# Kernel optimization log

Hardware: AMD Instinct MI355X
Metric: run time of the kernel (lower is better)

Reference implementation:

```python
import jax, jax.numpy as jnp
import numpy as np


def _patchify(x, p):
    # x: [B, V, H, W] -> [B, V, L, p*p] with L = (H/p)*(W/p), matching Conv2d(kernel=stride=p)
    B, V, H, W = x.shape
    hp, wp = H // p, W // p
    x = x.reshape(B, V, hp, p, wp, p)
    x = x.transpose(0, 1, 2, 4, 3, 5)  # [B, V, hp, wp, p, p]
    return x.reshape(B, V, hp * wp, p * p)


def setup_inputs() -> dict:
    key = jax.random.key(0)
    ks = jax.random.split(key, 12)
    B, V, H, W, p, D = 2, 16, 128, 256, 4, 1024
    L = (H // p) * (W // p)  # 2048
    std = 0.02
    return {
        "x": jax.random.normal(ks[0], (B, V, H, W), jnp.float32),
        "proj_w": jax.random.normal(ks[1], (V, D, p * p), jnp.float32) * std,
        "proj_b": jnp.zeros((V, D), jnp.float32),
        "channel_embed": jax.random.normal(ks[2], (1, V, D), jnp.float32) * std,
        "pos_embed": jax.random.normal(ks[3], (1, L, D), jnp.float32) * std,
        "channel_query": jax.random.normal(ks[4], (1, 1, D), jnp.float32) * std,
        "wq": jax.random.normal(ks[5], (D, D), jnp.float32) * std,
        "wk": jax.random.normal(ks[6], (D, D), jnp.float32) * std,
        "wv": jax.random.normal(ks[7], (D, D), jnp.float32) * std,
        "bq": jnp.zeros((D,), jnp.float32),
        "bk": jnp.zeros((D,), jnp.float32),
        "bv": jnp.zeros((D,), jnp.float32),
        "wo": jax.random.normal(ks[8], (D, D), jnp.float32) * std,
        "bo": jnp.zeros((D,), jnp.float32),
        "num_heads": 16,
    }


def reference(x, proj_w, proj_b, channel_embed, pos_embed, channel_query,
              wq, wk, wv, bq, bk, bv, wo, bo, num_heads):
    D = proj_w.shape[1]
    p = int(round(np.sqrt(proj_w.shape[-1])))
    nh = int(num_heads)
    dh = D // nh

    # per-variable patch embed (Conv2d k=stride=p == patch-matmul)
    patches = _patchify(x, p)                                   # [B, V, L, p*p]
    tok = jnp.einsum('bvlk,vdk->bvld', patches, proj_w)         # [B, V, L, D]
    tok = tok + proj_b[None, :, None, :]

    # add variable (channel) and positional embeddings
    tok = tok + channel_embed[:, :, None, :] + pos_embed[:, None, :, :]

    # aggregate_variables: single-query MHA over V, batched over B*L
    h = tok.transpose(0, 2, 1, 3)                               # [B, L, V, D]
    q = channel_query[0, 0] @ wq.T + bq                         # [D]
    qh = q.reshape(nh, dh)
    k = (jnp.einsum('blvd,ed->blve', h, wk) + bk).reshape(*h.shape[:3], nh, dh)
    v = (jnp.einsum('blvd,ed->blve', h, wv) + bv).reshape(*h.shape[:3], nh, dh)
    scores = jnp.einsum('he,blvhe->blhv', qh, k) / np.sqrt(dh)  # [B, L, nh, V]
    attn = jax.nn.softmax(scores, axis=-1)
    ctx = jnp.einsum('blhv,blvhe->blhe', attn, v)               # [B, L, nh, dh]
    ctx = ctx.reshape(h.shape[0], h.shape[1], D)
    out = ctx @ wo.T + bo                                       # [B, L, D]
    return out
```

## Files before the change

kernel.cpp:

```cpp
#include <hip/hip_runtime.h>
#include <hip/hip_bf16.h>

using bf16 = __hip_bfloat16;
using bf16x8 = __attribute__((ext_vector_type(8))) short;
using f32x4  = __attribute__((ext_vector_type(4))) float;

__device__ inline unsigned short f2bu(float f){ bf16 h = __float2bfloat16(f); return *(unsigned short*)&h; }
__device__ inline void async_cp16(const void* g, void* l){
  __builtin_amdgcn_global_load_lds((const __attribute__((address_space(1))) void*)g,
                                   (__attribute__((address_space(3))) void*)l, 16, 0, 0);
}
union BF8 { unsigned short s[8]; bf16x8 v; };

constexpr int D_ = 1024, L_ = 2048;
constexpr int CN = 384;

__device__ inline size_t w3idx(int row, int col){
  const int hh = row >> 6, m = row & 15, dt = (row >> 4) & 3;
  const int vp = col >> 5, quad = (col >> 3) & 3, j = col & 7;
  return (size_t)hh*18432 + vp*2048 + dt*512 + quad*128 + m*8 + j;
}

__global__ __launch_bounds__(256) void k_prep2(const float* __restrict__ wv, const float* __restrict__ wo,
                                               const float* __restrict__ pe,
                                               const float* __restrict__ proj_w, const float* __restrict__ proj_b,
                                               const float* __restrict__ ce, const float* __restrict__ cq,
                                               const float* __restrict__ wq, const float* __restrict__ bq,
                                               const float* __restrict__ wk,
                                               unsigned short* __restrict__ Ab, unsigned short* __restrict__ wo_b,
                                               unsigned short* __restrict__ pe_b,
                                               unsigned short* __restrict__ Btb){
  __shared__ float t[64][17];
  __shared__ float qL[64];
  __shared__ float red[4][64];
  const int blk = blockIdx.x;
  const int tid = threadIdx.x;
  if (blk < 4096){
    int i = blk*256 + tid;
    const float* src; unsigned short* dst; size_t off;
    if (i < 262144){ src = wv; dst = Ab;   off = i; }
    else if (i < 524288){ src = wo; dst = wo_b; off = i - 262144; }
    else           { src = pe; dst = pe_b; off = i - 524288; }
    float4 v = *(const float4*)(src + off*4);
    *(ushort4*)(dst + off*4) = make_ushort4(f2bu(v.x), f2bu(v.y), f2bu(v.z), f2bu(v.w));
  } else if (blk < 4352){
    const int r_ = blk - 4096;
    const int v = r_ >> 4, dd0 = (r_ & 15)*64;
    { const int r = tid >> 2, kq = tid & 3;
      float4 a = *(const float4*)(proj_w + ((size_t)(v*D_ + dd0 + r))*16 + kq*4);
      t[r][kq*4+0]=a.x; t[r][kq*4+1]=a.y; t[r][kq*4+2]=a.z; t[r][kq*4+3]=a.w; }
    __syncthreads();
    { const int k = tid >> 4, c0 = (tid & 15)*4;
      ushort4 o = make_ushort4(f2bu(t[c0+0][k]), f2bu(t[c0+1][k]), f2bu(t[c0+2][k]), f2bu(t[c0+3][k]));
      *(ushort4*)(Btb + (size_t)(v*16+k)*D_ + dd0 + c0) = o; }
    if (tid < 16){
      const int c0 = tid*4;
      float4 pb = *(const float4*)(proj_b + v*D_ + dd0 + c0);
      float4 cc = *(const float4*)(ce     + v*D_ + dd0 + c0);
      ushort4 o = make_ushort4(f2bu(pb.x+cc.x), f2bu(pb.y+cc.y), f2bu(pb.z+cc.z), f2bu(pb.w+cc.w));
      *(ushort4*)(Btb + (size_t)(256+v)*D_ + dd0 + c0) = o;
    }
  } else {
    const int b = blk - 4352;
    const int hh = b >> 4, dq = b & 15;
    const int wave = tid >> 6, lane = tid & 63;
    {
      float cqv[16];
      #pragma unroll
      for (int k=0;k<16;++k) cqv[k] = cq[lane + 64*k];
      #pragma unroll
      for (int j=0;j<16;++j){
        const int e = hh*64 + wave*16 + j;
        const float* wr = wq + (size_t)e*D_;
        float p = 0.f;
        #pragma unroll
        for (int k=0;k<16;++k) p += cqv[k]*wr[lane + 64*k];
        #pragma unroll
        for (int m=32;m>=1;m>>=1) p += __shfl_xor(p, m, 64);
        if (lane==0) qL[wave*16+j] = p + bq[e];
      }
    }
    __syncthreads();
    {
      const int eg = wave, dl = lane;
      const int d = dq*64 + dl;
      float s = 0.f;
      #pragma unroll
      for (int j=0;j<16;++j){
        int e = hh*64 + eg*16 + j;
        s += qL[eg*16+j]*wk[(size_t)e*D_ + d];
      }
      red[eg][dl] = s;
      __syncthreads();
      if (eg==0)
        Ab[(size_t)(1024+hh)*D_ + d] = f2bu(((red[0][dl]+red[1][dl]) + (red[2][dl]+red[3][dl]))*0.125f);
    }
  }
}

template<int MFRAG, bool BIAS, bool WB2>
__device__ inline void gemm_body(unsigned short* As, unsigned short* Bs,
                                 const unsigned short* __restrict__ Abf, const unsigned short* __restrict__ Bt,
                                 const float* __restrict__ bias, float* __restrict__ C,
                                 unsigned short* __restrict__ W, const float* __restrict__ bvp,
                                 int m0, int n0, int K, int ldc, int Mvalid){
  const int tid = threadIdx.x;
  const int wave = tid >> 6, lane = tid & 63;
  const int wm = wave & 1, wn = wave >> 1;
  const int lm = lane & 15, kg4 = lane >> 4;
  f32x4 acc[MFRAG][4];
  #pragma unroll
  for (int mf=0;mf<MFRAG;++mf)
    #pragma unroll
    for (int nf=0;nf<4;++nf) acc[mf][nf] = (f32x4){0.f,0.f,0.f,0.f};
  for (int k0=0; k0<K; k0+=64){
    #pragma unroll
    for (int i=0;i<MFRAG;++i){
      int idx = i*256 + tid;
      int row = idx >> 3, g = (idx & 7) ^ (row & 7);
      async_cp16(Abf + (size_t)(m0+row)*K + k0 + g*8, &As[idx*8]);
    }
    #pragma unroll
    for (int i=0;i<4;++i){
      int idx = i*256 + tid;
      int row = idx >> 3, g = (idx & 7) ^ (row & 7);
      async_cp16(Bt + (size_t)(n0+row)*K + k0 + g*8, &Bs[idx*8]);
    }
    __syncthreads();
    #pragma unroll
    for (int c=0;c<2;++c){
      bf16x8 af[MFRAG], bfr[4];
      #pragma unroll
      for (int f=0;f<MFRAG;++f){
        int row = wm*16*MFRAG + f*16 + lm;
        af[f] = *(const bf16x8*)(&As[row*64 + (((c*4+kg4) ^ (row&7)))*8]);
      }
      #pragma unroll
      for (int f=0;f<4;++f){
        int colr = wn*64 + f*16 + lm;
        bfr[f] = *(const bf16x8*)(&Bs[colr*64 + (((c*4+kg4) ^ (colr&7)))*8]);
      }
      #pragma unroll
      for (int mf=0;mf<MFRAG;++mf)
        #pragma unroll
        for (int nf=0;nf<4;++nf)
          acc[mf][nf] = __builtin_amdgcn_mfma_f32_16x16x32_bf16(af[mf], bfr[nf], acc[mf][nf], 0,0,0);
    }
    __syncthreads();
  }
  #pragma unroll
  for (int nf=0;nf<4;++nf){
    int col = n0 + wn*64 + nf*16 + lm;
    float bval = BIAS ? bias[col] : 0.f;
    #pragma unroll
    for (int mf=0;mf<MFRAG;++mf){
      #pragma unroll
      for (int r=0;r<4;++r){
        int row = m0 + wm*16*MFRAG + mf*16 + kg4*4 + r;
        if (row < Mvalid){
          float v = acc[mf][nf][r];
          C[(size_t)row*ldc + col] = v + bval;
          if (WB2 && row < 1024){
            if (col < 256)      W[w3idx(row,col)] = f2bu(v);
            else if (col < 272) W[w3idx(row,col)] = f2bu(v + bvp[row]);
            else if (col < 288) W[w3idx(row,col)] = 0;
          }
        }
      }
    }
  }
}

__global__ __launch_bounds__(256) void k_gemmCP2(const unsigned short* __restrict__ Ab,
                                                 const unsigned short* __restrict__ Btb,
                                                 const unsigned short* __restrict__ pe_b,
                                                 const float* __restrict__ bv,
                                                 float* __restrict__ Cbig, unsigned short* __restrict__ Wb2,
                                                 float* __restrict__ P2){
  __shared__ unsigned short As[64*64];
  __shared__ unsigned short Bs[128*64];
  if (blockIdx.x < 51){
    int bx = blockIdx.x % 3, by = blockIdx.x / 3;
    gemm_body<2,false,true>(As, Bs, Ab, Btb, nullptr, Cbig, Wb2, bv, by*64, bx*128, 1024, CN, 1040);
  } else {
    int b = blockIdx.x - 51;
    int bx = b & 7, by = b >> 3;
    gemm_body<1,false,false>(As, Bs, pe_b, Ab, nullptr, P2, nullptr, nullptr, by*32, bx*128, 1024, 1024, 2048);
  }
}

__global__ __launch_bounds__(256) void k_gemmOut(const unsigned short* __restrict__ ctxF,
                                                 const unsigned short* __restrict__ wo_b,
                                                 const float* __restrict__ bo, float* __restrict__ C){
  __shared__ unsigned short As[64*64];
  __shared__ unsigned short Bs[128*64];
  gemm_body<2,true,false>(As, Bs, ctxF, wo_b, bo, C, nullptr, nullptr,
                          blockIdx.y*64, blockIdx.x*128, 1024, 1024, 4096);
}

__global__ __launch_bounds__(256) void k_fused9(const float* __restrict__ x,
                                                const float* __restrict__ Cbig,
                                                const unsigned short* __restrict__ W3,
                                                const float* __restrict__ P2,
                                                unsigned short* __restrict__ ctxF){
  __shared__ float patchP[16*260];
  __shared__ float attnT[4*320];
  __shared__ __align__(16) unsigned short S[16*264];
  const int tid = threadIdx.x;
  const int bb  = blockIdx.x >> 9;
  const int sg  = (blockIdx.x >> 2) & 127;
  const int hqq = blockIdx.x & 3;
  unsigned short* ctx = ctxF + (size_t)bb*L_*D_;
  const int l0 = sg*16;
  {
    const int v = tid >> 4, u = tid & 15;
    const int hi = l0 >> 6, wi0 = l0 & 63;
    const float* xp = x + ((size_t)((bb*16+v)*128 + hi*4)*256 + (wi0+u)*4);
    float* dst = &patchP[u*260 + v*16];
    #pragma unroll
    for (int pi=0; pi<4; ++pi){
      float4 r = *(const float4*)(xp + pi*256);
      dst[pi*4+0]=r.x; dst[pi*4+1]=r.y; dst[pi*4+2]=r.z; dst[pi*4+3]=r.w;
    }
  }
  __syncthreads();
  if (tid < 64){
    const int s = tid >> 2, h4 = tid & 3;
    const int hh = hqq*4 + h4;
    const float* qrow = Cbig + (size_t)(1024+hh)*CN;
    const float* prow = &patchP[s*260];
    float4 qc0 = *(const float4*)(qrow+256);
    float4 qc1 = *(const float4*)(qrow+260);
    float4 qc2 = *(const float4*)(qrow+264);
    float4 qc3 = *(const float4*)(qrow+268);
    float qcv[16] = {qc0.x,qc0.y,qc0.z,qc0.w, qc1.x,qc1.y,qc1.z,qc1.w,
                     qc2.x,qc2.y,qc2.z,qc2.w, qc3.x,qc3.y,qc3.z,qc3.w};
    float sc[16];
    #pragma unroll
    for (int v=0; v<16; ++v){
      const float* qp = qrow + v*16;
      const float* pp = prow + v*16;
      float4 qa = *(const float4*)(qp+0),  qb = *(const float4*)(qp+4);
      float4 qc = *(const float4*)(qp+8),  qd = *(const float4*)(qp+12);
      float4 pa = *(const float4*)(pp+0),  pb2 = *(const float4*)(pp+4);
      float4 pc = *(const float4*)(pp+8),  pd = *(const float4*)(pp+12);
      float a = qcv[v];
      a += qa.x*pa.x + qa.y*pa.y + qa.z*pa.z + qa.w*pa.w;
      a += qb.x*pb2.x + qb.y*pb2.y + qb.z*pb2.z + qb.w*pb2.w;
      a += qc.x*pc.x + qc.y*pc.y + qc.z*pc.z + qc.w*pc.w;
      a += qd.x*pd.x + qd.y*pd.y + qd.z*pd.z + qd.w*pd.w;
      sc[v] = a;
    }
    float mx = sc[0];
    #pragma unroll
    for (int v=1;v<16;++v) mx = fmaxf(mx, sc[v]);
    float sum = 0.f;
    #pragma unroll
    for (int v=0;v<16;++v){ sc[v] = __expf(sc[v]-mx); sum += sc[v]; }
    float inv = 1.f/sum;
    float* arow = &attnT[h4*320 + s*20];
    #pragma unroll
    for (int v=0;v<16;++v) arow[v] = sc[v]*inv;
  }
  __syncthreads();
  const int wave = tid >> 6, lane = tid & 63;
  const int m = lane & 15, quad = lane >> 4;
  const int hh = hqq*4 + wave;
  const float* at = &attnT[wave*320];
  const unsigned short* wbase = W3 + (size_t)hh*18432 + lane*8;
  f32x4 acc[4];
  #pragma unroll
  for (int dt=0;dt<4;++dt) acc[dt] = (f32x4){0.f,0.f,0.f,0.f};
  #pragma unroll
  for (int vp=0; vp<9; ++vp){
    BF8 af;
    if (vp < 8){
      const int v = vp*2 + (quad>>1);
      const int k8 = (quad&1)*8;
      const float aw = at[m*20 + v];
      const float* pp = &patchP[m*260 + v*16 + k8];
      float4 p0 = *(const float4*)(pp+0);
      float4 p1 = *(const float4*)(pp+4);
      af.s[0]=f2bu(aw*p0.x); af.s[1]=f2bu(aw*p0.y); af.s[2]=f2bu(aw*p0.z); af.s[3]=f2bu(aw*p0.w);
      af.s[4]=f2bu(aw*p1.x); af.s[5]=f2bu(aw*p1.y); af.s[6]=f2bu(aw*p1.z); af.s[7]=f2bu(aw*p1.w);
    } else {
      #pragma unroll
      for (int j=0;j<8;++j)
        af.s[j] = (quad < 2) ? f2bu(at[m*20 + quad*8 + j]) : (unsigned short)0;
    }
    #pragma unroll
    for (int dt=0; dt<4; ++dt){
      const bf16x8 bf = *(const bf16x8*)(wbase + vp*2048 + dt*512);
      acc[dt] = __builtin_amdgcn_mfma_f32_16x16x32_bf16(af.v, bf, acc[dt], 0,0,0);
    }
  }
  const int dblk0 = wave*64;
  #pragma unroll
  for (int dt=0; dt<4; ++dt){
    const int d = hqq*256 + dblk0 + dt*16 + m;
    #pragma unroll
    for (int r=0;r<4;++r){
      const int s = quad*4 + r;
      S[s*264 + dblk0 + dt*16 + m] = f2bu(acc[dt][r] + P2[(size_t)(l0+s)*D_ + d]);
    }
  }
  __syncthreads();
  {
    const int row = tid >> 4, ch = tid & 15;
    const unsigned short* srcp = &S[row*264 + ch*16];
    unsigned short* dstp = ctx + (size_t)(l0+row)*D_ + hqq*256 + ch*16;
    *(uint4*)(dstp)   = *(const uint4*)(srcp);
    *(uint4*)(dstp+8) = *(const uint4*)(srcp+8);
  }
}

extern "C" void kernel_launch(void* const* d_in, const int* in_sizes, int n_in,
                              void* d_out, int out_size, void* d_ws, size_t ws_size,
                              hipStream_t stream){
  const float* x      = (const float*)d_in[0];
  const float* proj_w = (const float*)d_in[1];
  const float* proj_b = (const float*)d_in[2];
  const float* ce     = (const float*)d_in[3];
  const float* pe     = (const float*)d_in[4];
  const float* cq     = (const float*)d_in[5];
  const float* wq     = (const float*)d_in[6];
  const float* wk     = (const float*)d_in[7];
  const float* wv     = (const float*)d_in[8];
  const float* bq     = (const float*)d_in[9];
  const float* bv     = (const float*)d_in[11];
  const float* wo     = (const float*)d_in[12];
  const float* bo     = (const float*)d_in[13];
  float* out = (float*)d_out;

  char* base = (char*)d_ws;
  unsigned short* Ab   = (unsigned short*)(base);
  unsigned short* Btb  = (unsigned short*)(base + 2359296);
  float*          Cbig = (float*)(base + 3145728);
  unsigned short* wo_b = (unsigned short*)(base + 4743168);
  unsigned short* Wb2  = (unsigned short*)(base + 6840320);
  float*          P2   = (float*)(base + 7430144);
  unsigned short* ctxF = (unsigned short*)(base + 15818752);
  unsigned short* pe_b = (unsigned short*)(base + 24207360);

  k_prep2<<<4608, 256, 0, stream>>>(wv, wo, pe, proj_w, proj_b, ce, cq, wq, bq, wk, Ab, wo_b, pe_b, Btb);
  k_gemmCP2<<<563, 256, 0, stream>>>(Ab, Btb, pe_b, bv, Cbig, Wb2, P2);
  k_fused9<<<1024, 256, 0, stream>>>(x, Cbig, Wb2, P2, ctxF);
  k_gemmOut<<<dim3(8,64), 256, 0, stream>>>(ctxF, wo_b, bo, out);
}
```

Before: 173.8 us.

## Merge four head-quarter blocks into one 1024-thread block per token group

The fused attention kernel now runs one 1024-thread block per 16-token group covering all 16 heads, instead of four 256-thread blocks that each handled four heads. Each x patch tile is loaded once per group rather than four times, and every thread issues a single float4 load. The trade-off is a drop from 1024 to 256 blocks with larger shared-memory use per block. That may lower occupancy and leave only one block per CU on a 256-CU device.

```diff
diff --git a/kernel.cpp b/kernel.cpp
--- a/kernel.cpp
+++ b/kernel.cpp
@@ -198,36 +198,31 @@
                           blockIdx.y*64, blockIdx.x*128, 1024, 1024, 4096);
 }
 
-__global__ __launch_bounds__(256) void k_fused9(const float* __restrict__ x,
-                                                const float* __restrict__ Cbig,
-                                                const unsigned short* __restrict__ W3,
-                                                const float* __restrict__ P2,
-                                                unsigned short* __restrict__ ctxF){
+__global__ __launch_bounds__(1024) void k_fused10(const float* __restrict__ x,
+                                                  const float* __restrict__ Cbig,
+                                                  const unsigned short* __restrict__ W3,
+                                                  const float* __restrict__ P2,
+                                                  unsigned short* __restrict__ ctxF){
   __shared__ float patchP[16*260];
-  __shared__ float attnT[4*320];
-  __shared__ __align__(16) unsigned short S[16*264];
+  __shared__ float attnT[16*320];
+  __shared__ __align__(16) unsigned short S[16*1032];
   const int tid = threadIdx.x;
-  const int bb  = blockIdx.x >> 9;
-  const int sg  = (blockIdx.x >> 2) & 127;
-  const int hqq = blockIdx.x & 3;
+  const int bb  = blockIdx.x >> 7;
+  const int sg  = blockIdx.x & 127;
   unsigned short* ctx = ctxF + (size_t)bb*L_*D_;
   const int l0 = sg*16;
   {
-    const int v = tid >> 4, u = tid & 15;
+    const int u = tid & 15, pi = (tid >> 4) & 3, v = tid >> 6;
     const int hi = l0 >> 6, wi0 = l0 & 63;
-    const float* xp = x + ((size_t)((bb*16+v)*128 + hi*4)*256 + (wi0+u)*4);
-    float* dst = &patchP[u*260 + v*16];
-    #pragma unroll
-    for (int pi=0; pi<4; ++pi){
-      float4 r = *(const float4*)(xp + pi*256);
-      dst[pi*4+0]=r.x; dst[pi*4+1]=r.y; dst[pi*4+2]=r.z; dst[pi*4+3]=r.w;
-    }
+    const float* xp = x + ((size_t)((bb*16+v)*128 + hi*4 + pi)*256 + (wi0+u)*4);
+    float4 r = *(const float4*)xp;
+    float* dst = &patchP[u*260 + v*16 + pi*4];
+    dst[0]=r.x; dst[1]=r.y; dst[2]=r.z; dst[3]=r.w;
   }
   __syncthreads();
-  if (tid < 64){
-    const int s = tid >> 2, h4 = tid & 3;
-    const int hh = hqq*4 + h4;
-    const float* qrow = Cbig + (size_t)(1024+hh)*CN;
+  if (tid < 256){
+    const int s = tid >> 4, h = tid & 15;
+    const float* qrow = Cbig + (size_t)(1024+h)*CN;
     const float* prow = &patchP[s*260];
     float4 qc0 = *(const float4*)(qrow+256);
     float4 qc1 = *(const float4*)(qrow+260);
@@ -258,15 +253,15 @@
     #pragma unroll
     for (int v=0;v<16;++v){ sc[v] = __expf(sc[v]-mx); sum += sc[v]; }
     float inv = 1.f/sum;
-    float* arow = &attnT[h4*320 + s*20];
+    float* arow = &attnT[h*320 + s*20];
     #pragma unroll
     for (int v=0;v<16;++v) arow[v] = sc[v]*inv;
   }
   __syncthreads();
   const int wave = tid >> 6, lane = tid & 63;
   const int m = lane & 15, quad = lane >> 4;
-  const int hh = hqq*4 + wave;
-  const float* at = &attnT[wave*320];
+  const int hh = wave;
+  const float* at = &attnT[hh*320];
   const unsigned short* wbase = W3 + (size_t)hh*18432 + lane*8;
   f32x4 acc[4];
   #pragma unroll
@@ -294,21 +289,20 @@
       acc[dt] = __builtin_amdgcn_mfma_f32_16x16x32_bf16(af.v, bf, acc[dt], 0,0,0);
     }
   }
-  const int dblk0 = wave*64;
   #pragma unroll
   for (int dt=0; dt<4; ++dt){
-    const int d = hqq*256 + dblk0 + dt*16 + m;
+    const int d = hh*64 + dt*16 + m;
     #pragma unroll
     for (int r=0;r<4;++r){
       const int s = quad*4 + r;
-      S[s*264 + dblk0 + dt*16 + m] = f2bu(acc[dt][r] + P2[(size_t)(l0+s)*D_ + d]);
+      S[s*1032 + d] = f2bu(acc[dt][r] + P2[(size_t)(l0+s)*D_ + d]);
     }
   }
   __syncthreads();
   {
-    const int row = tid >> 4, ch = tid & 15;
-    const unsigned short* srcp = &S[row*264 + ch*16];
-    unsigned short* dstp = ctx + (size_t)(l0+row)*D_ + hqq*256 + ch*16;
+    const int row = tid >> 6, ch = tid & 63;
+    const unsigned short* srcp = &S[row*1032 + ch*16];
+    unsigned short* dstp = ctx + (size_t)(l0+row)*D_ + ch*16;
     *(uint4*)(dstp)   = *(const uint4*)(srcp);
     *(uint4*)(dstp+8) = *(const uint4*)(srcp+8);
   }
@@ -344,6 +338,6 @@
 
   k_prep2<<<4608, 256, 0, stream>>>(wv, wo, pe, proj_w, proj_b, ce, cq, wq, bq, wk, Ab, wo_b, pe_b, Btb);
   k_gemmCP2<<<563, 256, 0, stream>>>(Ab, Btb, pe_b, bv, Cbig, Wb2, P2);
-  k_fused9<<<1024, 256, 0, stream>>>(x, Cbig, Wb2, P2, ctxF);
+  k_fused10<<<256, 1024, 0, stream>>>(x, Cbig, Wb2, P2, ctxF);
   k_gemmOut<<<dim3(8,64), 256, 0, stream>>>(ctxF, wo_b, bo, out);
 }
```

Result: no change. 172.1 us (-1.0%).
